# Kernel tuning notes

Measured on AMD Instinct MI355X. Metric: run time of the kernel, lower is better.

The kernel has to match this reference:

```python
import jax, jax.numpy as jnp
import numpy as np

N_CELLS, IN_DIM, HID, OUT = 65536, 128, 256, 128
MLP_H = 128   # engine MLP hidden width is hard-coded to 128 in the source
N_MORPH = 32  # min(32, n_cells//4)


def setup_inputs() -> dict:
    key = jax.random.key(0)
    ks = jax.random.split(key, 18)
    s = 0.05
    return {
        "x": jax.random.normal(ks[0], (1, IN_DIM), jnp.float32),
        "hiddens": jax.random.normal(ks[1], (N_CELLS, HID), jnp.float32) * 0.1,
        "Wa1": jax.random.normal(ks[2], (MLP_H, IN_DIM + HID), jnp.float32) * s,
        "ba1": jax.random.normal(ks[3], (MLP_H,), jnp.float32) * s,
        "Wa2": jax.random.normal(ks[4], (OUT, MLP_H), jnp.float32) * s,
        "ba2": jax.random.normal(ks[5], (OUT,), jnp.float32) * s,
        "Wg1": jax.random.normal(ks[6], (MLP_H, IN_DIM + HID), jnp.float32) * s,
        "bg1": jax.random.normal(ks[7], (MLP_H,), jnp.float32) * s,
        "Wg2": jax.random.normal(ks[8], (OUT, MLP_H), jnp.float32) * s,
        "bg2": jax.random.normal(ks[9], (OUT,), jnp.float32) * s,
        "W_ih": jax.random.normal(ks[10], (3 * HID, OUT + 1), jnp.float32) * s,
        "W_hh": jax.random.normal(ks[11], (3 * HID, HID), jnp.float32) * s,
        "b_ih": jax.random.normal(ks[12], (3 * HID,), jnp.float32) * s,
        "b_hh": jax.random.normal(ks[13], (3 * HID,), jnp.float32) * s,
        "nat_w": jnp.eye(HID, dtype=jnp.float32),  # nn.init.eye_
        "morph_w": jax.random.normal(ks[14], (N_MORPH, HID, HID), jnp.float32) * 0.02,
        "morph_src": jax.random.randint(ks[15], (N_MORPH,), 0, N_CELLS, jnp.int32),
        "morph_tgt": jax.random.randint(ks[16], (N_MORPH,), 0, N_CELLS, jnp.int32),
        "step": 0,
    }


def _forward(x, hiddens, Wa1, ba1, Wa2, ba2, Wg1, bg1, Wg2, bg2,
             W_ih, W_hh, b_ih, b_hh, nat_w, morph_w, morph_src, morph_tgt, step):
    n = hiddens.shape[0]
    # --- BenchMind, batched over all cells (x broadcast to every cell) ---
    xb = jnp.broadcast_to(x, (n, x.shape[-1]))
    combined = jnp.concatenate([xb, hiddens], axis=-1)               # [n, in+hid]
    a = jax.nn.relu(combined @ Wa1.T + ba1) @ Wa2.T + ba2            # [n, out]
    g = jax.nn.relu(combined @ Wg1.T + bg1) @ Wg2.T + bg2            # [n, out]
    out = a - g                                                       # [n, out]
    tension = jnp.mean(out * out, axis=-1, keepdims=True)            # [n, 1]
    # mem_input is detached in torch
    mem_in = jax.lax.stop_gradient(jnp.concatenate([out, tension], axis=-1))
    # --- PyTorch GRUCell math ---
    gi = mem_in @ W_ih.T + b_ih                                      # [n, 3H]
    gh = hiddens @ W_hh.T + b_hh                                     # [n, 3H]
    i_r, i_z, i_n = jnp.split(gi, 3, axis=-1)
    h_r, h_z, h_n = jnp.split(gh, 3, axis=-1)
    r = jax.nn.sigmoid(i_r + h_r)
    z = jax.nn.sigmoid(i_z + h_z)
    nn_ = jnp.tanh(i_n + r * h_n)
    hid = jax.lax.stop_gradient((1.0 - z) * nn_ + z * hiddens)       # detached new hiddens
    if step % 3 == 0:
        hid = jax.lax.stop_gradient(hid @ nat_w.T)                   # natural transformation
    # --- limit / colimit (morphism gather-transform-aggregate) ---
    limit = jnp.einsum('mij,mj->i', morph_w, hid[morph_src]) / N_MORPH
    colimit = jnp.einsum('mji,mj->i', morph_w, hid[morph_tgt]) / N_MORPH
    diff = limit - colimit
    cat_tension = jnp.mean(diff * diff)
    hid = hid + 0.05 * jax.lax.stop_gradient(diff)[None, :]
    # --- faction sync (+ debate if step > 5) ---
    n_f = min(8, n // 2)
    fs = n // n_f
    hf = hid[: n_f * fs].reshape(n_f, fs, hid.shape[-1])
    fmean = hf.mean(axis=1, keepdims=True)                           # [n_f,1,H]
    hf = 0.85 * hf + 0.15 * fmean
    if step > 5:
        global_op = hf.mean(axis=1).mean(axis=0)                     # mean of faction means
        dc = max(1, fs // 4)
        hf = hf.at[:, :dc].set(0.85 * hf[:, :dc] + 0.15 * global_op)
    hid = jnp.concatenate([hf.reshape(n_f * fs, -1), hid[n_f * fs:]], axis=0)
    # --- tension-weighted combination (weights detached: .item() in torch) ---
    t = jax.lax.stop_gradient(tension[:, 0])                         # [n]
    w = jax.nn.softmax(t, axis=0)
    combined_out = jnp.sum(w[:, None] * out, axis=0, keepdims=True)  # [1, out]
    avg_tension = jnp.mean(tension) + 0.1 * cat_tension
    return combined_out, avg_tension, hid


def reference(x, hiddens, Wa1, ba1, Wa2, ba2, Wg1, bg1, Wg2, bg2,
              W_ih, W_hh, b_ih, b_hh, nat_w, morph_w, morph_src, morph_tgt, step):
    combined_out, avg_tension, _ = _forward(
        x, hiddens, Wa1, ba1, Wa2, ba2, Wg1, bg1, Wg2, bg2,
        W_ih, W_hh, b_ih, b_hh, nat_w, morph_w, morph_src, morph_tgt, step)
    return combined_out, avg_tension
```

## Files before the change

kernel.cpp:

```cpp
#include <hip/hip_runtime.h>
#include <math.h>

#define OFF_W1B   0
#define OFF_W2A   32768
#define OFF_XW1B  49152
#define OFF_B2D   49408
#define OFF_PT    49536
#define OFF_PE    51584
#define OFF_POUT  53632
#define OFF_MI4   315776
#define OFF_TEN   323968
#define OFF_HH4   324032
#define OFF_GI    340416
#define OFF_GH    389568
#define OFF_PLIM  438720
#define OFF_PCOL8 446912
#define OFF_GMSK  512448

typedef short bf16x8 __attribute__((ext_vector_type(8)));
typedef short s16x4  __attribute__((ext_vector_type(4)));
typedef float f32x4  __attribute__((ext_vector_type(4)));

__device__ __forceinline__ unsigned short f2bf(float f) {
    unsigned u = __builtin_bit_cast(unsigned, f);
    u += 0x7FFFu + ((u >> 16) & 1u);
    return (unsigned short)(u >> 16);
}

__device__ __forceinline__ bf16x8 cvt8(float4 a, float4 b) {
    bf16x8 v;
    v[0] = (short)f2bf(a.x); v[1] = (short)f2bf(a.y);
    v[2] = (short)f2bf(a.z); v[3] = (short)f2bf(a.w);
    v[4] = (short)f2bf(b.x); v[5] = (short)f2bf(b.y);
    v[6] = (short)f2bf(b.z); v[7] = (short)f2bf(b.w);
    return v;
}

__global__ __launch_bounds__(256) void k_prep(
    const float* __restrict__ x, const float* __restrict__ hiddens,
    const float* __restrict__ Wa1, const float* __restrict__ ba1,
    const float* __restrict__ Wa2, const float* __restrict__ ba2,
    const float* __restrict__ Wg1, const float* __restrict__ bg1,
    const float* __restrict__ Wg2, const float* __restrict__ bg2,
    const int* __restrict__ msrc, const int* __restrict__ mtgt,
    float* __restrict__ ws)
{
    const int b = blockIdx.x, t = threadIdx.x;
    unsigned short* w1b = (unsigned short*)(ws + OFF_W1B);
    unsigned short* w2a = (unsigned short*)(ws + OFF_W2A);
    if (b < 256) {
        const int n = b;
        const float* row = (n < 128) ? &Wa1[n * 384] : &Wg1[(n - 128) * 384];
        const int kc = t >> 3;
        w1b[(kc * 256 + n) * 8 + (t & 7)] = f2bf(row[128 + t]);
        if (n < 128) {
            float w2 = (t < 128) ? Wa2[n * 128 + t] : -Wg2[n * 128 + (t - 128)];
            w2a[(kc * 128 + n) * 8 + (t & 7)] = f2bf(w2);
        }
    } else if (b == 256) {
        const int n = t;
        const float* wr = (n < 128) ? &Wa1[n * 384] : &Wg1[(n - 128) * 384];
        float s = (n < 128) ? ba1[n] : bg1[n - 128];
        for (int j = 0; j < 128; ++j) s = fmaf(x[j], wr[j], s);
        ws[OFF_XW1B + n] = s;
        if (n < 128) ws[OFF_B2D + n] = ba2[n] - bg2[n];
    } else if (b == 257) {
        unsigned* gm = (unsigned*)(ws + OFF_GMSK);
        for (int i = t; i < 2048; i += 256) gm[i] = 0u;
        __syncthreads();
        if (t < 64) {
            const int cell = (t < 32) ? msrc[t] : mtgt[t - 32];
            atomicOr(&gm[cell >> 5], 1u << (cell & 31));
        }
    } else {
        const int g = b - 258;
        const int cell = (g < 32) ? msrc[g] : mtgt[g - 32];
        ws[OFF_HH4 + (t >> 2) * 256 + g * 4 + (t & 3)] = hiddens[(size_t)cell * 256 + t];
    }
}

__global__ __launch_bounds__(256, 2) void k_main(
    const float* __restrict__ hiddens,
    const int* __restrict__ msrc, const int* __restrict__ mtgt,
    float* __restrict__ ws)
{
    __shared__ __align__(16) short hB[32 * 256];
    __shared__ __align__(16) short h1B[32 * 256];
    __shared__ float part[128];
    __shared__ float e_sm[32], t_sm_[32];
    __shared__ int gid_sm[64];

    const int tid  = threadIdx.x;
    const int lane = tid & 63, wid = tid >> 6;
    const int l15 = lane & 15, l4 = lane >> 4;
    const int bt = blockIdx.x;

    if (tid < 64) gid_sm[tid] = (tid < 32) ? msrc[tid] : mtgt[tid - 32];

    const uint4* w1g = (const uint4*)(ws + OFF_W1B);
    const uint4* w2g = (const uint4*)(ws + OFF_W2A);
    const unsigned* gm = (const unsigned*)(ws + OFF_GMSK);

    {
        const int rc = tid >> 3;
        const float* hsrc = hiddens + (size_t)(bt * 32 + rc) * 256 + (tid & 7) * 32;
        float4 v0 = *(const float4*)(hsrc + 0);
        float4 v1 = *(const float4*)(hsrc + 4);
        float4 v2 = *(const float4*)(hsrc + 8);
        float4 v3 = *(const float4*)(hsrc + 12);
        float4 v4 = *(const float4*)(hsrc + 16);
        float4 v5 = *(const float4*)(hsrc + 20);
        float4 v6 = *(const float4*)(hsrc + 24);
        float4 v7 = *(const float4*)(hsrc + 28);
        const int kc0 = (tid & 7) * 4;
        *(bf16x8*)&hB[rc * 256 + (((kc0 + 0) ^ (rc & 15)) << 3)] = cvt8(v0, v1);
        *(bf16x8*)&hB[rc * 256 + (((kc0 + 1) ^ (rc & 15)) << 3)] = cvt8(v2, v3);
        *(bf16x8*)&hB[rc * 256 + (((kc0 + 2) ^ (rc & 15)) << 3)] = cvt8(v4, v5);
        *(bf16x8*)&hB[rc * 256 + (((kc0 + 3) ^ (rc & 15)) << 3)] = cvt8(v6, v7);
    }
    __syncthreads();

    const int wb1 = wid * 64 + l15;
    uint4 c0 = w1g[(0 + l4) * 256 + wb1 + 0];
    uint4 c1 = w1g[(0 + l4) * 256 + wb1 + 16];
    uint4 c2 = w1g[(0 + l4) * 256 + wb1 + 32];
    uint4 c3 = w1g[(0 + l4) * 256 + wb1 + 48];
    uint4 p0 = w1g[(4 + l4) * 256 + wb1 + 0];
    uint4 p1 = w1g[(4 + l4) * 256 + wb1 + 16];
    uint4 p2 = w1g[(4 + l4) * 256 + wb1 + 32];
    uint4 p3 = w1g[(4 + l4) * 256 + wb1 + 48];
    uint4 g2c0, g2c1, g2p0, g2p1;

    f32x4 acc[4][2];
#pragma unroll
    for (int q = 0; q < 4; ++q)
#pragma unroll
        for (int ct = 0; ct < 2; ++ct) acc[q][ct] = (f32x4)0.f;

    __builtin_amdgcn_s_setprio(1);
#pragma unroll
    for (int s = 0; s < 8; ++s) {
        uint4 f0, f1, f2, f3;
        if (s < 6) {
            f0 = w1g[((s + 2) * 4 + l4) * 256 + wb1 + 0];
            f1 = w1g[((s + 2) * 4 + l4) * 256 + wb1 + 16];
            f2 = w1g[((s + 2) * 4 + l4) * 256 + wb1 + 32];
            f3 = w1g[((s + 2) * 4 + l4) * 256 + wb1 + 48];
        } else if (s == 6) {
            g2c0 = w2g[(0 + l4) * 128 + wid * 32 + l15];
            g2c1 = w2g[(0 + l4) * 128 + wid * 32 + 16 + l15];
        } else {
            g2p0 = w2g[(4 + l4) * 128 + wid * 32 + l15];
            g2p1 = w2g[(4 + l4) * 128 + wid * 32 + 16 + l15];
        }
        bf16x8 bfr0 = *(const bf16x8*)&hB[(0 * 16 + l15) * 256 + (((s * 4 + l4) ^ l15) << 3)];
        bf16x8 bfr1 = *(const bf16x8*)&hB[(1 * 16 + l15) * 256 + (((s * 4 + l4) ^ l15) << 3)];
        acc[0][0] = __builtin_amdgcn_mfma_f32_16x16x32_bf16(__builtin_bit_cast(bf16x8, c0), bfr0, acc[0][0], 0, 0, 0);
        acc[0][1] = __builtin_amdgcn_mfma_f32_16x16x32_bf16(__builtin_bit_cast(bf16x8, c0), bfr1, acc[0][1], 0, 0, 0);
        acc[1][0] = __builtin_amdgcn_mfma_f32_16x16x32_bf16(__builtin_bit_cast(bf16x8, c1), bfr0, acc[1][0], 0, 0, 0);
        acc[1][1] = __builtin_amdgcn_mfma_f32_16x16x32_bf16(__builtin_bit_cast(bf16x8, c1), bfr1, acc[1][1], 0, 0, 0);
        acc[2][0] = __builtin_amdgcn_mfma_f32_16x16x32_bf16(__builtin_bit_cast(bf16x8, c2), bfr0, acc[2][0], 0, 0, 0);
        acc[2][1] = __builtin_amdgcn_mfma_f32_16x16x32_bf16(__builtin_bit_cast(bf16x8, c2), bfr1, acc[2][1], 0, 0, 0);
        acc[3][0] = __builtin_amdgcn_mfma_f32_16x16x32_bf16(__builtin_bit_cast(bf16x8, c3), bfr0, acc[3][0], 0, 0, 0);
        acc[3][1] = __builtin_amdgcn_mfma_f32_16x16x32_bf16(__builtin_bit_cast(bf16x8, c3), bfr1, acc[3][1], 0, 0, 0);
        c0 = p0; c1 = p1; c2 = p2; c3 = p3;
        if (s < 6) { p0 = f0; p1 = f1; p2 = f2; p3 = f3; }
    }
    __builtin_amdgcn_s_setprio(0);

#pragma unroll
    for (int nt = 0; nt < 4; ++nt) {
        const int n0 = wid * 64 + nt * 16 + l4 * 4;
        float4 xb = *(const float4*)(ws + OFF_XW1B + n0);
        const float bx[4] = {xb.x, xb.y, xb.z, xb.w};
        const int chunk = n0 >> 3;
        const int off = (l4 & 1) * 4;
#pragma unroll
        for (int ct = 0; ct < 2; ++ct) {
            const int c = ct * 16 + l15;
            s16x4 pk;
#pragma unroll
            for (int r = 0; r < 4; ++r)
                pk[r] = (short)f2bf(fmaxf(acc[nt][ct][r] + bx[r], 0.f));
            *(s16x4*)&h1B[c * 256 + ((chunk ^ l15) << 3) + off] = pk;
        }
    }
    __syncthreads();

    f32x4 acc2[2][2];
#pragma unroll
    for (int ot = 0; ot < 2; ++ot)
#pragma unroll
        for (int ct = 0; ct < 2; ++ct) acc2[ot][ct] = (f32x4)0.f;

    __builtin_amdgcn_s_setprio(1);
#pragma unroll
    for (int s = 0; s < 8; ++s) {
        uint4 f0, f1;
        if (s < 6) {
            f0 = w2g[((s + 2) * 4 + l4) * 128 + wid * 32 + l15];
            f1 = w2g[((s + 2) * 4 + l4) * 128 + wid * 32 + 16 + l15];
        }
        bf16x8 b20 = *(const bf16x8*)&h1B[(0 * 16 + l15) * 256 + (((s * 4 + l4) ^ l15) << 3)];
        bf16x8 b21 = *(const bf16x8*)&h1B[(1 * 16 + l15) * 256 + (((s * 4 + l4) ^ l15) << 3)];
        acc2[0][0] = __builtin_amdgcn_mfma_f32_16x16x32_bf16(__builtin_bit_cast(bf16x8, g2c0), b20, acc2[0][0], 0, 0, 0);
        acc2[0][1] = __builtin_amdgcn_mfma_f32_16x16x32_bf16(__builtin_bit_cast(bf16x8, g2c0), b21, acc2[0][1], 0, 0, 0);
        acc2[1][0] = __builtin_amdgcn_mfma_f32_16x16x32_bf16(__builtin_bit_cast(bf16x8, g2c1), b20, acc2[1][0], 0, 0, 0);
        acc2[1][1] = __builtin_amdgcn_mfma_f32_16x16x32_bf16(__builtin_bit_cast(bf16x8, g2c1), b21, acc2[1][1], 0, 0, 0);
        g2c0 = g2p0; g2c1 = g2p1;
        if (s < 6) { g2p0 = f0; g2p1 = f1; }
    }
    __builtin_amdgcn_s_setprio(0);

    float outv[2][2][4];
#pragma unroll
    for (int ot = 0; ot < 2; ++ot) {
        float4 bd = *(const float4*)(ws + OFF_B2D + wid * 32 + ot * 16 + l4 * 4);
        const float bv[4] = {bd.x, bd.y, bd.z, bd.w};
#pragma unroll
        for (int ct = 0; ct < 2; ++ct)
#pragma unroll
            for (int r = 0; r < 4; ++r)
                outv[ot][ct][r] = acc2[ot][ct][r] + bv[r];
    }

#pragma unroll
    for (int ct = 0; ct < 2; ++ct) {
        float sq = 0.f;
#pragma unroll
        for (int ot = 0; ot < 2; ++ot)
#pragma unroll
            for (int r = 0; r < 4; ++r)
                sq = fmaf(outv[ot][ct][r], outv[ot][ct][r], sq);
        sq += __shfl_xor(sq, 16);
        sq += __shfl_xor(sq, 32);
        if (l4 == 0) part[wid * 32 + ct * 16 + l15] = sq;
    }
    __syncthreads();

    if (tid < 32) {
        float s = part[tid] + part[32 + tid] + part[64 + tid] + part[96 + tid];
        const float tv = s * (1.f / 128.f);
        const float ev = expf(tv);
        t_sm_[tid] = tv; e_sm[tid] = ev;
        float pt = tv, pe = ev;
        for (int off = 16; off > 0; off >>= 1) {
            pt += __shfl_down(pt, off);
            pe += __shfl_down(pe, off);
        }
        if (tid == 0) { ws[OFF_PT + bt] = pt; ws[OFF_PE + bt] = pe; }
        unsigned m = gm[bt];
        while (m) {
            const int g = __builtin_ctz(m); m &= m - 1;
            const int cg = gid_sm[g];
            if ((cg >> 5) == bt && (cg & 31) == tid) ws[OFF_TEN + g] = tv;
        }
    }
    __syncthreads();

    {
        float p[2][4];
#pragma unroll
        for (int ot = 0; ot < 2; ++ot)
#pragma unroll
            for (int r = 0; r < 4; ++r) {
                float s = e_sm[l15] * outv[ot][0][r];
                s = fmaf(e_sm[16 + l15], outv[ot][1][r], s);
                p[ot][r] = s;
            }
#pragma unroll
        for (int ot = 0; ot < 2; ++ot)
#pragma unroll
            for (int r = 0; r < 4; ++r) {
                p[ot][r] += __shfl_xor(p[ot][r], 1);
                p[ot][r] += __shfl_xor(p[ot][r], 2);
                p[ot][r] += __shfl_xor(p[ot][r], 4);
                p[ot][r] += __shfl_xor(p[ot][r], 8);
            }
        if (l15 == 0) {
#pragma unroll
            for (int ot = 0; ot < 2; ++ot)
                *(float4*)(ws + OFF_POUT + (size_t)bt * 128 + wid * 32 + ot * 16 + l4 * 4) =
                    make_float4(p[ot][0], p[ot][1], p[ot][2], p[ot][3]);
        }
    }
    {
        unsigned m = gm[bt];
        while (m) {
            const int g = __builtin_ctz(m); m &= m - 1;
            const int cg = gid_sm[g];
            if ((cg >> 5) != bt) continue;
            const int c = cg & 31;
            if ((c & 15) == l15) {
                const int ct = c >> 4;
#pragma unroll
                for (int ot = 0; ot < 2; ++ot)
                    *(float4*)(ws + OFF_MI4 + (wid * 8 + ot * 4 + l4) * 256 + g * 4) =
                        make_float4(outv[ot][ct][0], outv[ot][ct][1],
                                    outv[ot][ct][2], outv[ot][ct][3]);
            }
        }
    }
}

__global__ __launch_bounds__(256) void k_tail1(
    const float* __restrict__ W_ih, const float* __restrict__ W_hh,
    const float* __restrict__ b_ih, const float* __restrict__ b_hh,
    float* __restrict__ ws)
{
    const int lane = threadIdx.x & 63;
    const int w    = threadIdx.x >> 6;
    const int row  = __builtin_amdgcn_readfirstlane(blockIdx.x * 4 + w);
    const float* mi4 = ws + OFF_MI4;
    const float* hh4 = ws + OFF_HH4;

    const float* wi = W_ih + row * 129;
    float gi = b_ih[row];
#pragma unroll 8
    for (int q = 0; q < 32; ++q) {
        float4 a = *(const float4*)(mi4 + q * 256 + lane * 4);
        gi = fmaf(wi[4 * q + 0], a.x, gi);
        gi = fmaf(wi[4 * q + 1], a.y, gi);
        gi = fmaf(wi[4 * q + 2], a.z, gi);
        gi = fmaf(wi[4 * q + 3], a.w, gi);
    }
    gi = fmaf(ws[OFF_TEN + lane], wi[128], gi);

    const float* wh = W_hh + (size_t)row * 256;
    float gh = b_hh[row];
#pragma unroll 8
    for (int q = 0; q < 64; ++q) {
        float4 a = *(const float4*)(hh4 + q * 256 + lane * 4);
        float4 b = *(const float4*)(wh + 4 * q);
        gh = fmaf(b.x, a.x, gh);
        gh = fmaf(b.y, a.y, gh);
        gh = fmaf(b.z, a.z, gh);
        gh = fmaf(b.w, a.w, gh);
    }
    ws[OFF_GI + lane * 768 + row] = gi;
    ws[OFF_GH + lane * 768 + row] = gh;
}

__global__ __launch_bounds__(256) void k_morph(
    const float* __restrict__ morph_w, const float* __restrict__ nat_w,
    const int* __restrict__ step, float* __restrict__ ws)
{
    __shared__ float wsm[32 * 264];
    __shared__ float hd0[256], hd1[256];
    __shared__ float hs[256], ht[256];
    const int blk = blockIdx.x, t = threadIdx.x;
    const int m = blk >> 3, ch = blk & 7;
    const float* wm = morph_w + (size_t)m * 65536 + (size_t)ch * 32 * 256;
    {
        const int r = t >> 3, c0 = (t & 7) * 32;
#pragma unroll
        for (int it = 0; it < 8; ++it)
            *(float4*)&wsm[r * 264 + c0 + it * 4] = *(const float4*)(wm + r * 256 + c0 + it * 4);
    }
#pragma unroll
    for (int h = 0; h < 2; ++h) {
        const int g = h * 32 + m;
        const float i_r = ws[OFF_GI + g * 768 + t];
        const float i_z = ws[OFF_GI + g * 768 + 256 + t];
        const float i_n = ws[OFF_GI + g * 768 + 512 + t];
        const float h_r = ws[OFF_GH + g * 768 + t];
        const float h_z = ws[OFF_GH + g * 768 + 256 + t];
        const float h_n = ws[OFF_GH + g * 768 + 512 + t];
        const float hv  = ws[OFF_HH4 + (t >> 2) * 256 + g * 4 + (t & 3)];
        const float r  = 1.f / (1.f + expf(-(i_r + h_r)));
        const float z  = 1.f / (1.f + expf(-(i_z + h_z)));
        const float nn = tanhf(i_n + r * h_n);
        const float hid = (1.f - z) * nn + z * hv;
        if (h == 0) hd0[t] = hid; else hd1[t] = hid;
    }
    __syncthreads();

    float hn0, hn1;
    if (step[0] % 3 == 0) {
        const float4* wr = (const float4*)(nat_w + (size_t)t * 256);
        float s0 = 0.f, s1 = 0.f;
        for (int q = 0; q < 64; ++q) {
            float4 wq = wr[q];
            s0 = fmaf(wq.x, hd0[4 * q + 0], s0); s1 = fmaf(wq.x, hd1[4 * q + 0], s1);
            s0 = fmaf(wq.y, hd0[4 * q + 1], s0); s1 = fmaf(wq.y, hd1[4 * q + 1], s1);
            s0 = fmaf(wq.z, hd0[4 * q + 2], s0); s1 = fmaf(wq.z, hd1[4 * q + 2], s1);
            s0 = fmaf(wq.w, hd0[4 * q + 3], s0); s1 = fmaf(wq.w, hd1[4 * q + 3], s1);
        }
        hn0 = s0; hn1 = s1;
    } else {
        hn0 = hd0[t]; hn1 = hd1[t];
    }
    hs[t] = hn0; ht[t] = hn1;
    __syncthreads();

    {
        const int il = t >> 3, jc = t & 7;
        float L = 0.f;
#pragma unroll 8
        for (int jj = 0; jj < 32; ++jj) {
            const int j = jc + 8 * jj;
            L = fmaf(wsm[il * 264 + j], hs[j], L);
        }
        L += __shfl_down(L, 4);
        L += __shfl_down(L, 2);
        L += __shfl_down(L, 1);
        if (jc == 0) ws[OFF_PLIM + m * 256 + ch * 32 + il] = L;
    }
    {
        float C = 0.f;
#pragma unroll 8
        for (int r = 0; r < 32; ++r)
            C = fmaf(wsm[r * 264 + t], ht[ch * 32 + r], C);
        ws[OFF_PCOL8 + blk * 256 + t] = C;
    }
}

__global__ __launch_bounds__(256) void k_out(const float* __restrict__ ws,
                                             float* __restrict__ out)
{
    __shared__ float red[256];
    const int b = blockIdx.x, t = threadIdx.x;
    if (b < 128) {
        float so = 0.f, se = 0.f;
        for (int i = t; i < 2048; i += 256) {
            so += ws[OFF_POUT + (size_t)i * 128 + b];
            se += ws[OFF_PE + i];
        }
        red[t] = so; __syncthreads();
        for (int s = 128; s > 0; s >>= 1) { if (t < s) red[t] += red[t + s]; __syncthreads(); }
        const float SO = red[0]; __syncthreads();
        red[t] = se; __syncthreads();
        for (int s = 128; s > 0; s >>= 1) { if (t < s) red[t] += red[t + s]; __syncthreads(); }
        if (t == 0) out[b] = SO / red[0];
    } else {
        float pt = 0.f;
        for (int i = t; i < 2048; i += 256) pt += ws[OFF_PT + i];
        float L = 0.f, C = 0.f;
        for (int m = 0; m < 32; ++m) L += ws[OFF_PLIM + m * 256 + t];
        for (int mc = 0; mc < 256; ++mc) C += ws[OFF_PCOL8 + mc * 256 + t];
        const float d = (L - C) * (1.f / 32.f);
        red[t] = d * d; __syncthreads();
        for (int s = 128; s > 0; s >>= 1) { if (t < s) red[t] += red[t + s]; __syncthreads(); }
        const float cat = red[0] * (1.f / 256.f); __syncthreads();
        red[t] = pt; __syncthreads();
        for (int s = 128; s > 0; s >>= 1) { if (t < s) red[t] += red[t + s]; __syncthreads(); }
        if (t == 0) out[128] = red[0] * (1.f / 65536.f) + 0.1f * cat;
    }
}

extern "C" void kernel_launch(void* const* d_in, const int* in_sizes, int n_in,
                              void* d_out, int out_size, void* d_ws, size_t ws_size,
                              hipStream_t stream)
{
    const float* x     = (const float*)d_in[0];
    const float* hidd  = (const float*)d_in[1];
    const float* Wa1   = (const float*)d_in[2];
    const float* ba1   = (const float*)d_in[3];
    const float* Wa2   = (const float*)d_in[4];
    const float* ba2   = (const float*)d_in[5];
    const float* Wg1   = (const float*)d_in[6];
    const float* bg1   = (const float*)d_in[7];
    const float* Wg2   = (const float*)d_in[8];
    const float* bg2   = (const float*)d_in[9];
    const float* W_ih  = (const float*)d_in[10];
    const float* W_hh  = (const float*)d_in[11];
    const float* b_ih  = (const float*)d_in[12];
    const float* b_hh  = (const float*)d_in[13];
    const float* nat_w = (const float*)d_in[14];
    const float* mw    = (const float*)d_in[15];
    const int*   msrc  = (const int*)d_in[16];
    const int*   mtgt  = (const int*)d_in[17];
    const int*   step  = (const int*)d_in[18];

    float* out = (float*)d_out;
    float* ws  = (float*)d_ws;

    k_prep <<<322, 256, 0, stream>>>(x, hidd, Wa1, ba1, Wa2, ba2, Wg1, bg1, Wg2, bg2, msrc, mtgt, ws);
    k_main <<<2048, 256, 0, stream>>>(hidd, msrc, mtgt, ws);
    k_tail1<<<192, 256, 0, stream>>>(W_ih, W_hh, b_ih, b_hh, ws);
    k_morph<<<256, 256, 0, stream>>>(mw, nat_w, step, ws);
    k_out  <<<129, 256, 0, stream>>>(ws, out);
}
```

Before: 76.17 us.

## Fuse tail GRU, morph and output kernels with grid-wide atomic barriers

Merges k_tail1, k_morph and k_out into a single 256-block kernel. Grid-wide atomic counters with spin-waits stand in for the kernel boundaries. The output-column reductions run in the spare blocks during the GRU phase, and block 0 does the final scalar reduction. This removes two launch gaps, but it depends on all 256 blocks being resident at once and adds spin-wait overhead.

Measured after the change: 102.2 us. +34.2%, slower.

```diff
diff --git a/kernel.cpp b/kernel.cpp
--- a/kernel.cpp
+++ b/kernel.cpp
@@ -16,6 +16,7 @@
 #define OFF_PLIM  438720
 #define OFF_PCOL8 446912
 #define OFF_GMSK  512448
+#define OFF_SYNC  514496
 
 typedef short bf16x8 __attribute__((ext_vector_type(8)));
 typedef short s16x4  __attribute__((ext_vector_type(4)));
@@ -67,6 +68,7 @@
     } else if (b == 257) {
         unsigned* gm = (unsigned*)(ws + OFF_GMSK);
         for (int i = t; i < 2048; i += 256) gm[i] = 0u;
+        if (t < 4) ((unsigned*)(ws + OFF_SYNC))[t] = 0u;
         __syncthreads();
         if (t < 64) {
             const int cell = (t < 32) ? msrc[t] : mtgt[t - 32];
@@ -303,136 +305,154 @@
     }
 }
 
-__global__ __launch_bounds__(256) void k_tail1(
+__global__ __launch_bounds__(256) void k_tail_all(
     const float* __restrict__ W_ih, const float* __restrict__ W_hh,
     const float* __restrict__ b_ih, const float* __restrict__ b_hh,
-    float* __restrict__ ws)
-{
-    const int lane = threadIdx.x & 63;
-    const int w    = threadIdx.x >> 6;
-    const int row  = __builtin_amdgcn_readfirstlane(blockIdx.x * 4 + w);
-    const float* mi4 = ws + OFF_MI4;
-    const float* hh4 = ws + OFF_HH4;
-
-    const float* wi = W_ih + row * 129;
-    float gi = b_ih[row];
-#pragma unroll 8
-    for (int q = 0; q < 32; ++q) {
-        float4 a = *(const float4*)(mi4 + q * 256 + lane * 4);
-        gi = fmaf(wi[4 * q + 0], a.x, gi);
-        gi = fmaf(wi[4 * q + 1], a.y, gi);
-        gi = fmaf(wi[4 * q + 2], a.z, gi);
-        gi = fmaf(wi[4 * q + 3], a.w, gi);
-    }
-    gi = fmaf(ws[OFF_TEN + lane], wi[128], gi);
-
-    const float* wh = W_hh + (size_t)row * 256;
-    float gh = b_hh[row];
-#pragma unroll 8
-    for (int q = 0; q < 64; ++q) {
-        float4 a = *(const float4*)(hh4 + q * 256 + lane * 4);
-        float4 b = *(const float4*)(wh + 4 * q);
-        gh = fmaf(b.x, a.x, gh);
-        gh = fmaf(b.y, a.y, gh);
-        gh = fmaf(b.z, a.z, gh);
-        gh = fmaf(b.w, a.w, gh);
-    }
-    ws[OFF_GI + lane * 768 + row] = gi;
-    ws[OFF_GH + lane * 768 + row] = gh;
-}
-
-__global__ __launch_bounds__(256) void k_morph(
-    const float* __restrict__ morph_w, const float* __restrict__ nat_w,
-    const int* __restrict__ step, float* __restrict__ ws)
+    const float* __restrict__ nat_w, const float* __restrict__ morph_w,
+    const int* __restrict__ step,
+    float* __restrict__ ws, float* __restrict__ out)
 {
     __shared__ float wsm[32 * 264];
-    __shared__ float hd0[256], hd1[256];
-    __shared__ float hs[256], ht[256];
-    const int blk = blockIdx.x, t = threadIdx.x;
-    const int m = blk >> 3, ch = blk & 7;
-    const float* wm = morph_w + (size_t)m * 65536 + (size_t)ch * 32 * 256;
-    {
-        const int r = t >> 3, c0 = (t & 7) * 32;
-#pragma unroll
-        for (int it = 0; it < 8; ++it)
-            *(float4*)&wsm[r * 264 + c0 + it * 4] = *(const float4*)(wm + r * 256 + c0 + it * 4);
-    }
-#pragma unroll
-    for (int h = 0; h < 2; ++h) {
-        const int g = h * 32 + m;
-        const float i_r = ws[OFF_GI + g * 768 + t];
-        const float i_z = ws[OFF_GI + g * 768 + 256 + t];
-        const float i_n = ws[OFF_GI + g * 768 + 512 + t];
-        const float h_r = ws[OFF_GH + g * 768 + t];
-        const float h_z = ws[OFF_GH + g * 768 + 256 + t];
-        const float h_n = ws[OFF_GH + g * 768 + 512 + t];
-        const float hv  = ws[OFF_HH4 + (t >> 2) * 256 + g * 4 + (t & 3)];
-        const float r  = 1.f / (1.f + expf(-(i_r + h_r)));
-        const float z  = 1.f / (1.f + expf(-(i_z + h_z)));
-        const float nn = tanhf(i_n + r * h_n);
-        const float hid = (1.f - z) * nn + z * hv;
-        if (h == 0) hd0[t] = hid; else hd1[t] = hid;
-    }
-    __syncthreads();
-
-    float hn0, hn1;
-    if (step[0] % 3 == 0) {
-        const float4* wr = (const float4*)(nat_w + (size_t)t * 256);
-        float s0 = 0.f, s1 = 0.f;
-        for (int q = 0; q < 64; ++q) {
-            float4 wq = wr[q];
-            s0 = fmaf(wq.x, hd0[4 * q + 0], s0); s1 = fmaf(wq.x, hd1[4 * q + 0], s1);
-            s0 = fmaf(wq.y, hd0[4 * q + 1], s0); s1 = fmaf(wq.y, hd1[4 * q + 1], s1);
-            s0 = fmaf(wq.z, hd0[4 * q + 2], s0); s1 = fmaf(wq.z, hd1[4 * q + 2], s1);
-            s0 = fmaf(wq.w, hd0[4 * q + 3], s0); s1 = fmaf(wq.w, hd1[4 * q + 3], s1);
-        }
-        hn0 = s0; hn1 = s1;
-    } else {
-        hn0 = hd0[t]; hn1 = hd1[t];
-    }
-    hs[t] = hn0; ht[t] = hn1;
-    __syncthreads();
-
-    {
-        const int il = t >> 3, jc = t & 7;
-        float L = 0.f;
-#pragma unroll 8
-        for (int jj = 0; jj < 32; ++jj) {
-            const int j = jc + 8 * jj;
-            L = fmaf(wsm[il * 264 + j], hs[j], L);
-        }
-        L += __shfl_down(L, 4);
-        L += __shfl_down(L, 2);
-        L += __shfl_down(L, 1);
-        if (jc == 0) ws[OFF_PLIM + m * 256 + ch * 32 + il] = L;
-    }
-    {
-        float C = 0.f;
-#pragma unroll 8
-        for (int r = 0; r < 32; ++r)
-            C = fmaf(wsm[r * 264 + t], ht[ch * 32 + r], C);
-        ws[OFF_PCOL8 + blk * 256 + t] = C;
-    }
-}
-
-__global__ __launch_bounds__(256) void k_out(const float* __restrict__ ws,
-                                             float* __restrict__ out)
-{
+    __shared__ float hd0[256], hd1[256], hs[256], ht[256];
     __shared__ float red[256];
     const int b = blockIdx.x, t = threadIdx.x;
-    if (b < 128) {
-        float so = 0.f, se = 0.f;
-        for (int i = t; i < 2048; i += 256) {
-            so += ws[OFF_POUT + (size_t)i * 128 + b];
-            se += ws[OFF_PE + i];
-        }
-        red[t] = so; __syncthreads();
-        for (int s = 128; s > 0; s >>= 1) { if (t < s) red[t] += red[t + s]; __syncthreads(); }
-        const float SO = red[0]; __syncthreads();
-        red[t] = se; __syncthreads();
-        for (int s = 128; s > 0; s >>= 1) { if (t < s) red[t] += red[t + s]; __syncthreads(); }
-        if (t == 0) out[b] = SO / red[0];
+    unsigned* sync = (unsigned*)(ws + OFF_SYNC);
+
+    if (b < 192) {
+        const int lane = t & 63;
+        const int w    = t >> 6;
+        const int row  = __builtin_amdgcn_readfirstlane(b * 4 + w);
+        const float* mi4 = ws + OFF_MI4;
+        const float* hh4 = ws + OFF_HH4;
+
+        const float* wi = W_ih + row * 129;
+        float gi = b_ih[row];
+#pragma unroll 8
+        for (int q = 0; q < 32; ++q) {
+            float4 a = *(const float4*)(mi4 + q * 256 + lane * 4);
+            gi = fmaf(wi[4 * q + 0], a.x, gi);
+            gi = fmaf(wi[4 * q + 1], a.y, gi);
+            gi = fmaf(wi[4 * q + 2], a.z, gi);
+            gi = fmaf(wi[4 * q + 3], a.w, gi);
+        }
+        gi = fmaf(ws[OFF_TEN + lane], wi[128], gi);
+
+        const float* wh = W_hh + (size_t)row * 256;
+        float gh = b_hh[row];
+#pragma unroll 8
+        for (int q = 0; q < 64; ++q) {
+            float4 a = *(const float4*)(hh4 + q * 256 + lane * 4);
+            float4 bb = *(const float4*)(wh + 4 * q);
+            gh = fmaf(bb.x, a.x, gh);
+            gh = fmaf(bb.y, a.y, gh);
+            gh = fmaf(bb.z, a.z, gh);
+            gh = fmaf(bb.w, a.w, gh);
+        }
+        ws[OFF_GI + lane * 768 + row] = gi;
+        ws[OFF_GH + lane * 768 + row] = gh;
     } else {
+#pragma unroll
+        for (int cc = 0; cc < 2; ++cc) {
+            const int col = (b - 192) * 2 + cc;
+            float so = 0.f, se = 0.f;
+            for (int i = t; i < 2048; i += 256) {
+                so += ws[OFF_POUT + (size_t)i * 128 + col];
+                se += ws[OFF_PE + i];
+            }
+            red[t] = so; __syncthreads();
+            for (int s = 128; s > 0; s >>= 1) { if (t < s) red[t] += red[t + s]; __syncthreads(); }
+            const float SO = red[0]; __syncthreads();
+            red[t] = se; __syncthreads();
+            for (int s = 128; s > 0; s >>= 1) { if (t < s) red[t] += red[t + s]; __syncthreads(); }
+            if (t == 0) out[col] = SO / red[0];
+            __syncthreads();
+        }
+    }
+
+    __syncthreads();
+    if (t == 0) {
+        __hip_atomic_fetch_add(&sync[0], 1u, __ATOMIC_RELEASE, __HIP_MEMORY_SCOPE_AGENT);
+        while (__hip_atomic_load(&sync[0], __ATOMIC_ACQUIRE, __HIP_MEMORY_SCOPE_AGENT) < 256u)
+            __builtin_amdgcn_s_sleep(2);
+    }
+    __syncthreads();
+
+    {
+        const int m = b >> 3, ch = b & 7;
+        const float* wm = morph_w + (size_t)m * 65536 + (size_t)ch * 32 * 256;
+        {
+            const int r = t >> 3, c0 = (t & 7) * 32;
+#pragma unroll
+            for (int it = 0; it < 8; ++it)
+                *(float4*)&wsm[r * 264 + c0 + it * 4] = *(const float4*)(wm + r * 256 + c0 + it * 4);
+        }
+#pragma unroll
+        for (int h = 0; h < 2; ++h) {
+            const int g = h * 32 + m;
+            const float i_r = ws[OFF_GI + g * 768 + t];
+            const float i_z = ws[OFF_GI + g * 768 + 256 + t];
+            const float i_n = ws[OFF_GI + g * 768 + 512 + t];
+            const float h_r = ws[OFF_GH + g * 768 + t];
+            const float h_z = ws[OFF_GH + g * 768 + 256 + t];
+            const float h_n = ws[OFF_GH + g * 768 + 512 + t];
+            const float hv  = ws[OFF_HH4 + (t >> 2) * 256 + g * 4 + (t & 3)];
+            const float r  = 1.f / (1.f + expf(-(i_r + h_r)));
+            const float z  = 1.f / (1.f + expf(-(i_z + h_z)));
+            const float nn = tanhf(i_n + r * h_n);
+            const float hid = (1.f - z) * nn + z * hv;
+            if (h == 0) hd0[t] = hid; else hd1[t] = hid;
+        }
+        __syncthreads();
+
+        float hn0, hn1;
+        if (step[0] % 3 == 0) {
+            const float4* wr = (const float4*)(nat_w + (size_t)t * 256);
+            float s0 = 0.f, s1 = 0.f;
+            for (int q = 0; q < 64; ++q) {
+                float4 wq = wr[q];
+                s0 = fmaf(wq.x, hd0[4 * q + 0], s0); s1 = fmaf(wq.x, hd1[4 * q + 0], s1);
+                s0 = fmaf(wq.y, hd0[4 * q + 1], s0); s1 = fmaf(wq.y, hd1[4 * q + 1], s1);
+                s0 = fmaf(wq.z, hd0[4 * q + 2], s0); s1 = fmaf(wq.z, hd1[4 * q + 2], s1);
+                s0 = fmaf(wq.w, hd0[4 * q + 3], s0); s1 = fmaf(wq.w, hd1[4 * q + 3], s1);
+            }
+            hn0 = s0; hn1 = s1;
+        } else {
+            hn0 = hd0[t]; hn1 = hd1[t];
+        }
+        hs[t] = hn0; ht[t] = hn1;
+        __syncthreads();
+
+        {
+            const int il = t >> 3, jc = t & 7;
+            float L = 0.f;
+#pragma unroll 8
+            for (int jj = 0; jj < 32; ++jj) {
+                const int j = jc + 8 * jj;
+                L = fmaf(wsm[il * 264 + j], hs[j], L);
+            }
+            L += __shfl_down(L, 4);
+            L += __shfl_down(L, 2);
+            L += __shfl_down(L, 1);
+            if (jc == 0) ws[OFF_PLIM + m * 256 + ch * 32 + il] = L;
+        }
+        {
+            float C = 0.f;
+#pragma unroll 8
+            for (int r = 0; r < 32; ++r)
+                C = fmaf(wsm[r * 264 + t], ht[ch * 32 + r], C);
+            ws[OFF_PCOL8 + b * 256 + t] = C;
+        }
+    }
+
+    __syncthreads();
+    if (t == 0)
+        __hip_atomic_fetch_add(&sync[1], 1u, __ATOMIC_RELEASE, __HIP_MEMORY_SCOPE_AGENT);
+    if (b == 0) {
+        if (t == 0) {
+            while (__hip_atomic_load(&sync[1], __ATOMIC_ACQUIRE, __HIP_MEMORY_SCOPE_AGENT) < 256u)
+                __builtin_amdgcn_s_sleep(2);
+        }
+        __syncthreads();
         float pt = 0.f;
         for (int i = t; i < 2048; i += 256) pt += ws[OFF_PT + i];
         float L = 0.f, C = 0.f;
@@ -475,9 +495,7 @@
     float* out = (float*)d_out;
     float* ws  = (float*)d_ws;
 
-    k_prep <<<322, 256, 0, stream>>>(x, hidd, Wa1, ba1, Wa2, ba2, Wg1, bg1, Wg2, bg2, msrc, mtgt, ws);
-    k_main <<<2048, 256, 0, stream>>>(hidd, msrc, mtgt, ws);
-    k_tail1<<<192, 256, 0, stream>>>(W_ih, W_hh, b_ih, b_hh, ws);
-    k_morph<<<256, 256, 0, stream>>>(mw, nat_w, step, ws);
-    k_out  <<<129, 256, 0, stream>>>(ws, out);
+    k_prep    <<<322, 256, 0, stream>>>(x, hidd, Wa1, ba1, Wa2, ba2, Wg1, bg1, Wg2, bg2, msrc, mtgt, ws);
+    k_main    <<<2048, 256, 0, stream>>>(hidd, msrc, mtgt, ws);
+    k_tail_all<<<256, 256, 0, stream>>>(W_ih, W_hh, b_ih, b_hh, nat_w, mw, step, ws, out);
 }
```
